# Optimization experiments

Measured on AMD Instinct MI355X. Metric: run time of the kernel, lower is better.

## Reference

```python
import jax, jax.numpy as jnp
import numpy as np

D_MODEL = 1024
N_HEAD = 16
D_K = D_MODEL // N_HEAD


def setup_inputs() -> dict:
    key = jax.random.key(0)
    ks = jax.random.split(key, 11)
    B, T = 2, 2048
    s = 1.0 / np.sqrt(D_MODEL)
    return {
        "q": jax.random.normal(ks[0], (B, T, D_MODEL), jnp.float32),
        "k": jax.random.normal(ks[1], (B, T, D_MODEL), jnp.float32),
        "v": jax.random.normal(ks[2], (B, T, D_MODEL), jnp.float32),
        "w_q": jax.random.normal(ks[3], (D_MODEL, D_MODEL), jnp.float32) * s,
        "b_q": jax.random.normal(ks[4], (D_MODEL,), jnp.float32) * 0.01,
        "w_k": jax.random.normal(ks[5], (D_MODEL, D_MODEL), jnp.float32) * s,
        "b_k": jax.random.normal(ks[6], (D_MODEL,), jnp.float32) * 0.01,
        "w_v": jax.random.normal(ks[7], (D_MODEL, D_MODEL), jnp.float32) * s,
        "b_v": jax.random.normal(ks[8], (D_MODEL,), jnp.float32) * 0.01,
        "w_o": jax.random.normal(ks[9], (D_MODEL, D_MODEL), jnp.float32) * s,
        "b_o": jax.random.normal(ks[10], (D_MODEL,), jnp.float32) * 0.01,
    }


def reference(q, k, v, w_q, b_q, w_k, b_k, w_v, b_v, w_o, b_o):
    B, T, _ = q.shape
    # QKV projections -> [B, H, T, d_k]
    def proj(x, w, b):
        return (jnp.einsum('btd,de->bte', x, w) + b).reshape(B, T, N_HEAD, D_K).transpose(0, 2, 1, 3)
    qh = proj(q, w_q, b_q)
    kh = proj(k, w_k, b_k)
    vh = proj(v, w_v, b_v)
    scale = jnp.float32(1.0 / np.sqrt(D_K))
    scores = jnp.einsum('bhqd,bhkd->bhqk', qh, kh) * scale  # [B,H,T,T]
    attn = jax.nn.softmax(scores, axis=-1)
    # dropout is identity in eval mode
    out = jnp.einsum('bhqk,bhkd->bhqd', attn, vh)  # [B,H,T,d_k]
    out = out.transpose(0, 2, 1, 3).reshape(B, T, N_HEAD * D_K)
    return jnp.einsum('btd,de->bte', out, w_o) + b_o
```

## Files before the change

### kernel.cpp

```cpp
#include <hip/hip_runtime.h>
#include <stdint.h>

#define DEVI static __device__ __forceinline__

typedef float f32x4 __attribute__((ext_vector_type(4)));
typedef float f32x16 __attribute__((ext_vector_type(16)));
typedef short s16x8 __attribute__((ext_vector_type(8)));
typedef unsigned short u16x4 __attribute__((ext_vector_type(4)));
typedef uint32_t u32x2 __attribute__((ext_vector_type(2)));
typedef uint32_t u32x4 __attribute__((ext_vector_type(4)));

DEVI unsigned short f2bf(float f) {
  union { float f; uint32_t u; } v; v.f = f;
  uint32_t u = v.u;
  return (unsigned short)((u + 0x7fffu + ((u >> 16) & 1u)) >> 16);
}

DEVI uint32_t cvtpk(float lo, float hi) {
  uint32_t r;
  asm("v_cvt_pk_bf16_f32 %0, %1, %2" : "=v"(r) : "v"(lo), "v"(hi));
  return r;
}

DEVI void pl32swap(uint32_t& a, uint32_t& b) {
#if __has_builtin(__builtin_amdgcn_permlane32_swap)
  u32x2 r = __builtin_amdgcn_permlane32_swap(a, b, false, false);
  a = r[0]; b = r[1];
#else
  asm("v_permlane32_swap_b32 %0, %1" : "+v"(a), "+v"(b));
#endif
}

DEVI void g2l16(const void* g, void* l) {
  __builtin_amdgcn_global_load_lds(
      (const __attribute__((address_space(1))) void*)g,
      (__attribute__((address_space(3))) void*)l, 16, 0, 0);
}

__global__ __launch_bounds__(256) void k_cvt3(const float* __restrict__ q,
                                              const float* __restrict__ k,
                                              const float* __restrict__ v,
                                              unsigned short* __restrict__ out) {
  const int y = blockIdx.y;
  const float* in = y == 0 ? q : y == 1 ? k : v;
  unsigned short* o = out + (size_t)y * 4194304;
  int idx = blockIdx.x * blockDim.x + threadIdx.x;
  int stride = gridDim.x * blockDim.x;
  for (int i = idx * 4; i < 4194304; i += stride * 4) {
    f32x4 x = *(const f32x4*)(in + i);
    u16x4 r;
    for (int j = 0; j < 4; ++j) r[j] = f2bf(x[j]);
    *(u16x4*)(o + i) = r;
  }
}

__global__ __launch_bounds__(256) void k_wt4(const float* w0, const float* w1,
                                             const float* w2, const float* w3,
                                             unsigned short* t0, unsigned short* t1,
                                             unsigned short* t2, unsigned short* t3) {
  const int z = blockIdx.z;
  const float* w = z == 0 ? w0 : z == 1 ? w1 : z == 2 ? w2 : w3;
  unsigned short* wt = z == 0 ? t0 : z == 1 ? t1 : z == 2 ? t2 : t3;
  __shared__ float tile[32][33];
  const int tx = threadIdx.x, ty = threadIdx.y;
  const int n0 = blockIdx.x * 32, k0 = blockIdx.y * 32;
  for (int j = 0; j < 4; ++j)
    tile[ty + j * 8][tx] = w[(size_t)(k0 + ty + j * 8) * 1024 + n0 + tx];
  __syncthreads();
  for (int j = 0; j < 4; ++j)
    wt[(size_t)(n0 + ty + j * 8) * 1024 + k0 + tx] = f2bf(tile[tx][ty + j * 8]);
}

__global__ __launch_bounds__(256) void k_gemm_multi(
    const unsigned short* A0, const unsigned short* A1, const unsigned short* A2,
    const unsigned short* B0, const unsigned short* B1, const unsigned short* B2,
    const float* c0, const float* c1, const float* c2,
    void* o0, void* o1, void* o2, int mode0) {
  constexpr int K = 1024;
  const int z = blockIdx.y;
  const unsigned short* A = z == 0 ? A0 : z == 1 ? A1 : A2;
  const unsigned short* Bt = z == 0 ? B0 : z == 1 ? B1 : B2;
  const float* bias = z == 0 ? c0 : z == 1 ? c1 : c2;
  void* outp = z == 0 ? o0 : z == 1 ? o1 : o2;
  const int MODE = mode0 + z;

  __shared__ __align__(16) unsigned short As[128 * 64];
  __shared__ __align__(16) unsigned short Bs[64 * 64];
  const int tid = threadIdx.x;
  const int lane = tid & 63, w = tid >> 6;
  const int g = lane >> 4, c = lane & 15;
  const int bm = blockIdx.x >> 4, bn = blockIdx.x & 15;
  const int m0 = bm * 128, n0 = bn * 64;
  const int wr = w >> 1, wc = w & 1;
  f32x4 acc[4][2] = {};

  for (int kt = 0; kt < 16; ++kt) {
    const int k0 = kt * 64;
    __syncthreads();
    for (int it = 0; it < 4; ++it) {
      int e = it * 256 + tid;
      int row = e >> 3, cwp = (e & 7) ^ (row & 7);
      g2l16(A + (size_t)(m0 + row) * K + k0 + cwp * 8,
            (char*)As + (it * 256 + (w << 6)) * 16);
    }
    for (int it = 0; it < 2; ++it) {
      int e = it * 256 + tid;
      int row = e >> 3, cwp = (e & 7) ^ (row & 7);
      g2l16(Bt + (size_t)(n0 + row) * K + k0 + cwp * 8,
            (char*)Bs + (it * 256 + (w << 6)) * 16);
    }
    __syncthreads();
    for (int kk = 0; kk < 2; ++kk) {
      s16x8 af[4], bfr[2];
      for (int mi = 0; mi < 4; ++mi) {
        int row = wr * 64 + mi * 16 + c;
        int ch = (kk * 4 + g) ^ (row & 7);
        af[mi] = *(const s16x8*)((const char*)As + row * 128 + ch * 16);
      }
      for (int ni = 0; ni < 2; ++ni) {
        int row = wc * 32 + ni * 16 + c;
        int ch = (kk * 4 + g) ^ (row & 7);
        bfr[ni] = *(const s16x8*)((const char*)Bs + row * 128 + ch * 16);
      }
      for (int mi = 0; mi < 4; ++mi)
        for (int ni = 0; ni < 2; ++ni)
          acc[mi][ni] = __builtin_amdgcn_mfma_f32_16x16x32_bf16(
              af[mi], bfr[ni], acc[mi][ni], 0, 0, 0);
    }
  }

  if (MODE == 0 || MODE == 1) {
    unsigned short* out = (unsigned short*)outp;
    const float scale = (MODE == 0) ? 0.1803368801111204f : 1.0f;
    for (int mi = 0; mi < 4; ++mi)
      for (int ni = 0; ni < 2; ++ni) {
        int row = m0 + wr * 64 + mi * 16 + g * 4;
        int col = n0 + wc * 32 + ni * 16 + c;
        float bb = bias[col];
        for (int r = 0; r < 4; ++r)
          out[(size_t)(row + r) * 1024 + col] = f2bf((acc[mi][ni][r] + bb) * scale);
      }
  } else if (MODE == 2) {
    unsigned short* vt = (unsigned short*)outp;
    const int bq = m0 >> 11, t0 = m0 & 2047;
    for (int mi = 0; mi < 4; ++mi)
      for (int ni = 0; ni < 2; ++ni) {
        int rowb = wr * 64 + mi * 16 + g * 4;
        int coll = wc * 32 + ni * 16 + c;
        float bb = bias[n0 + coll];
        u16x4 pk;
        for (int r = 0; r < 4; ++r) pk[r] = f2bf(acc[mi][ni][r] + bb);
        *(u16x4*)(vt + (size_t)(bq * 1024 + n0 + coll) * 2048 + t0 + rowb) = pk;
      }
  } else {
    float* out = (float*)outp;
    for (int mi = 0; mi < 4; ++mi)
      for (int ni = 0; ni < 2; ++ni) {
        int row = m0 + wr * 64 + mi * 16 + g * 4;
        int col = n0 + wc * 32 + ni * 16 + c;
        float bb = bias[col];
        for (int r = 0; r < 4; ++r)
          out[(size_t)(row + r) * 1024 + col] = acc[mi][ni][r] + bb;
      }
  }
}

__global__ __launch_bounds__(256) void k_attn(const unsigned short* __restrict__ Qp,
                                              const unsigned short* __restrict__ Kp,
                                              const unsigned short* __restrict__ Vt,
                                              unsigned short* __restrict__ Att) {
  __shared__ __align__(16) unsigned short Ks[2][4096];
  __shared__ __align__(16) unsigned short Vs[2][4096];
  const int tid = threadIdx.x;
  const int lane = tid & 63, w = tid >> 6;
  const int l31 = lane & 31, hi = lane >> 5;
  const int blk = (blockIdx.x & 7) * 64 + (blockIdx.x >> 3);
  const int qt = blk & 15, bh = blk >> 4;
  const int b = bh >> 4, h = bh & 15;
  const int m0 = qt * 128 + w * 32;
  const size_t qkBase = (size_t)b * 2048 * 1024 + (size_t)h * 64;
  const size_t vtBase = ((size_t)b * 1024 + h * 64) * 2048;

  const unsigned short* qrow = Qp + qkBase + (size_t)(m0 + l31) * 1024;
  s16x8 bq[4];
#pragma unroll
  for (int s = 0; s < 4; ++s)
    bq[s] = *(const s16x8*)(qrow + s * 16 + hi * 8);

  const int srow = tid >> 2;
  const unsigned short* kg = Kp + qkBase + (size_t)srow * 1024 + (tid & 3) * 16;
  const unsigned short* vg = Vt + vtBase + (size_t)srow * 2048 + (tid & 3) * 16;
  const int wof0 = srow * 128 + ((((tid & 3) * 2 + 0) ^ (srow & 7)) * 16);
  const int wof1 = srow * 128 + ((((tid & 3) * 2 + 1) ^ (srow & 7)) * 16);

  float m_run = -1e30f, l_run = 0.f;
  f32x16 o0 = {}, o1 = {};

  {
    s16x8 k0 = *(const s16x8*)(kg), k1 = *(const s16x8*)(kg + 8);
    s16x8 v0 = *(const s16x8*)(vg), v1 = *(const s16x8*)(vg + 8);
    *(s16x8*)((char*)&Ks[0][0] + wof0) = k0;
    *(s16x8*)((char*)&Ks[0][0] + wof1) = k1;
    *(s16x8*)((char*)&Vs[0][0] + wof0) = v0;
    *(s16x8*)((char*)&Vs[0][0] + wof1) = v1;
  }
  __syncthreads();

  const int rch = l31 & 7;

#pragma unroll 1
  for (int t = 0; t < 32; ++t) {
    const int cur = t & 1;
    s16x8 k0, k1, v0, v1;
    if (t < 31) {
      const unsigned short* kgt = kg + (size_t)(t + 1) * 64 * 1024;
      const unsigned short* vgt = vg + (t + 1) * 64;
      k0 = *(const s16x8*)(kgt);
      k1 = *(const s16x8*)(kgt + 8);
      v0 = *(const s16x8*)(vgt);
      v1 = *(const s16x8*)(vgt + 8);
    }
    const char* ks = (const char*)&Ks[cur][0];
    const char* vs = (const char*)&Vs[cur][0];

    f32x16 s0 = {}, s1 = {};
    __builtin_amdgcn_s_setprio(1);
#pragma unroll
    for (int ds = 0; ds < 4; ++ds) {
      int ch = (2 * ds + hi) ^ rch;
      s16x8 a0 = *(const s16x8*)(ks + l31 * 128 + ch * 16);
      s16x8 a1 = *(const s16x8*)(ks + (32 + l31) * 128 + ch * 16);
      s0 = __builtin_amdgcn_mfma_f32_32x32x16_bf16(a0, bq[ds], s0, 0, 0, 0);
      s1 = __builtin_amdgcn_mfma_f32_32x32x16_bf16(a1, bq[ds], s1, 0, 0, 0);
    }
    __builtin_amdgcn_s_setprio(0);

    float tm = s0[0];
#pragma unroll
    for (int j = 1; j < 16; ++j) tm = fmaxf(tm, s0[j]);
#pragma unroll
    for (int j = 0; j < 16; ++j) tm = fmaxf(tm, s1[j]);
    tm = fmaxf(tm, __shfl_xor(tm, 32));
    if (!__all(tm - m_run <= 8.0f)) {
      float mt = fmaxf(m_run, tm);
      float al = exp2f(m_run - mt);
      l_run *= al;
#pragma unroll
      for (int j = 0; j < 16; ++j) { o0[j] *= al; o1[j] *= al; }
      m_run = mt;
    }
    float rs = 0.f;
#pragma unroll
    for (int j = 0; j < 16; ++j) { float p = exp2f(s0[j] - m_run); s0[j] = p; rs += p; }
#pragma unroll
    for (int j = 0; j < 16; ++j) { float p = exp2f(s1[j] - m_run); s1[j] = p; rs += p; }
    rs += __shfl_xor(rs, 32);
    l_run += rs;

    s16x8 pf[4];
    {
      uint32_t w0 = cvtpk(s0[0], s0[1]), w1 = cvtpk(s0[2], s0[3]);
      uint32_t w2 = cvtpk(s0[4], s0[5]), w3 = cvtpk(s0[6], s0[7]);
      uint32_t w4 = cvtpk(s0[8], s0[9]), w5 = cvtpk(s0[10], s0[11]);
      uint32_t w6 = cvtpk(s0[12], s0[13]), w7 = cvtpk(s0[14], s0[15]);
      pl32swap(w0, w2); pl32swap(w1, w3); pl32swap(w4, w6); pl32swap(w5, w7);
      u32x4 f0 = {w0, w1, w2, w3}, f1 = {w4, w5, w6, w7};
      pf[0] = *(s16x8*)&f0;
      pf[1] = *(s16x8*)&f1;
    }
    {
      uint32_t w0 = cvtpk(s1[0], s1[1]), w1 = cvtpk(s1[2], s1[3]);
      uint32_t w2 = cvtpk(s1[4], s1[5]), w3 = cvtpk(s1[6], s1[7]);
      uint32_t w4 = cvtpk(s1[8], s1[9]), w5 = cvtpk(s1[10], s1[11]);
      uint32_t w6 = cvtpk(s1[12], s1[13]), w7 = cvtpk(s1[14], s1[15]);
      pl32swap(w0, w2); pl32swap(w1, w3); pl32swap(w4, w6); pl32swap(w5, w7);
      u32x4 f0 = {w0, w1, w2, w3}, f1 = {w4, w5, w6, w7};
      pf[2] = *(s16x8*)&f0;
      pf[3] = *(s16x8*)&f1;
    }

    __builtin_amdgcn_s_setprio(1);
#pragma unroll
    for (int ksp = 0; ksp < 4; ++ksp) {
      int ch = (2 * ksp + hi) ^ rch;
      s16x8 a0 = *(const s16x8*)(vs + l31 * 128 + ch * 16);
      s16x8 a1 = *(const s16x8*)(vs + (32 + l31) * 128 + ch * 16);
      o0 = __builtin_amdgcn_mfma_f32_32x32x16_bf16(a0, pf[ksp], o0, 0, 0, 0);
      o1 = __builtin_amdgcn_mfma_f32_32x32x16_bf16(a1, pf[ksp], o1, 0, 0, 0);
    }
    __builtin_amdgcn_s_setprio(0);

    if (t < 31) {
      const int nb = cur ^ 1;
      *(s16x8*)((char*)&Ks[nb][0] + wof0) = k0;
      *(s16x8*)((char*)&Ks[nb][0] + wof1) = k1;
      *(s16x8*)((char*)&Vs[nb][0] + wof0) = v0;
      *(s16x8*)((char*)&Vs[nb][0] + wof1) = v1;
    }
    __syncthreads();
  }

  float inv = 1.0f / l_run;
  unsigned short* arow = Att + ((size_t)b * 2048 + m0 + l31) * 1024 + h * 64;
#pragma unroll
  for (int dblk = 0; dblk < 2; ++dblk) {
#pragma unroll
    for (int rq = 0; rq < 4; ++rq) {
      float e0 = (dblk ? o1[rq * 4 + 0] : o0[rq * 4 + 0]) * inv;
      float e1 = (dblk ? o1[rq * 4 + 1] : o0[rq * 4 + 1]) * inv;
      float e2 = (dblk ? o1[rq * 4 + 2] : o0[rq * 4 + 2]) * inv;
      float e3 = (dblk ? o1[rq * 4 + 3] : o0[rq * 4 + 3]) * inv;
      u32x2 pk;
      pk[0] = cvtpk(e0, e1);
      pk[1] = cvtpk(e2, e3);
      *(u32x2*)(arow + dblk * 32 + 8 * rq + 4 * hi) = pk;
    }
  }
}

extern "C" void kernel_launch(void* const* d_in, const int* in_sizes, int n_in,
                              void* d_out, int out_size, void* d_ws, size_t ws_size,
                              hipStream_t stream) {
  const float* q = (const float*)d_in[0];
  const float* k = (const float*)d_in[1];
  const float* v = (const float*)d_in[2];
  const float* w_q = (const float*)d_in[3];
  const float* b_q = (const float*)d_in[4];
  const float* w_k = (const float*)d_in[5];
  const float* b_k = (const float*)d_in[6];
  const float* w_v = (const float*)d_in[7];
  const float* b_v = (const float*)d_in[8];
  const float* w_o = (const float*)d_in[9];
  const float* b_o = (const float*)d_in[10];

  unsigned short* s = (unsigned short*)d_ws;
  unsigned short* qbf = s;
  unsigned short* kbf = s + 4194304;
  unsigned short* vbf = s + 8388608;
  unsigned short* wqT = s + 12582912;
  unsigned short* wkT = s + 13631488;
  unsigned short* wvT = s + 14680064;
  unsigned short* woT = s + 15728640;
  unsigned short* Qp  = s + 16777216;
  unsigned short* Kp  = s + 20971520;
  unsigned short* Vt  = s + 25165824;
  unsigned short* Att = qbf;

  k_cvt3<<<dim3(1024, 3), 256, 0, stream>>>(q, k, v, qbf);

  k_wt4<<<dim3(32, 32, 4), dim3(32, 8), 0, stream>>>(w_q, w_k, w_v, w_o,
                                                     wqT, wkT, wvT, woT);

  k_gemm_multi<<<dim3(512, 3), 256, 0, stream>>>(
      qbf, kbf, vbf, wqT, wkT, wvT, b_q, b_k, b_v,
      (void*)Qp, (void*)Kp, (void*)Vt, 0);

  k_attn<<<512, 256, 0, stream>>>(Qp, Kp, Vt, Att);

  k_gemm_multi<<<dim3(512, 1), 256, 0, stream>>>(
      Att, Att, Att, woT, woT, woT, b_o, b_o, b_o,
      d_out, d_out, d_out, 3);
}
```

Measured before the change: 143.7 us.

## Fuse fp32-to-bf16 input conversion into QKV GEMM and halve attention block size

Removes the separate q/k/v conversion kernel by having the QKV GEMM load fp32 activations directly, convert them to bf16 in registers and store them into swizzled LDS. This drops one launch and a full write and re-read of the bf16 copies. It loses the async global-to-LDS path for A and re-reads fp32 once per N-tile. The attention kernel now runs 128-thread blocks over 64 query rows with twice as many blocks, each thread loading more K/V per tile. Softmax row sums are reduced across the half-wave once at the end via permlane swap, and the max/sum reductions use tree form.

```diff
diff --git a/kernel.cpp b/kernel.cpp
--- a/kernel.cpp
+++ b/kernel.cpp
@@ -31,27 +31,32 @@
 #endif
 }
 
+DEVI float swap_half(float x, int hi) {
+  uint32_t a = __float_as_uint(x), b = a;
+  pl32swap(a, b);
+  return hi ? __uint_as_float(a) : __uint_as_float(b);
+}
+
 DEVI void g2l16(const void* g, void* l) {
   __builtin_amdgcn_global_load_lds(
       (const __attribute__((address_space(1))) void*)g,
       (__attribute__((address_space(3))) void*)l, 16, 0, 0);
 }
 
-__global__ __launch_bounds__(256) void k_cvt3(const float* __restrict__ q,
-                                              const float* __restrict__ k,
-                                              const float* __restrict__ v,
-                                              unsigned short* __restrict__ out) {
-  const int y = blockIdx.y;
-  const float* in = y == 0 ? q : y == 1 ? k : v;
-  unsigned short* o = out + (size_t)y * 4194304;
-  int idx = blockIdx.x * blockDim.x + threadIdx.x;
-  int stride = gridDim.x * blockDim.x;
-  for (int i = idx * 4; i < 4194304; i += stride * 4) {
-    f32x4 x = *(const f32x4*)(in + i);
-    u16x4 r;
-    for (int j = 0; j < 4; ++j) r[j] = f2bf(x[j]);
-    *(u16x4*)(o + i) = r;
-  }
+DEVI float vmax16(const f32x16& v) {
+  float a = fmaxf(fmaxf(v[0], v[1]), fmaxf(v[2], v[3]));
+  float b = fmaxf(fmaxf(v[4], v[5]), fmaxf(v[6], v[7]));
+  float c = fmaxf(fmaxf(v[8], v[9]), fmaxf(v[10], v[11]));
+  float d = fmaxf(fmaxf(v[12], v[13]), fmaxf(v[14], v[15]));
+  return fmaxf(fmaxf(a, b), fmaxf(c, d));
+}
+
+DEVI float vsum16(const f32x16& v) {
+  float a = (v[0] + v[1]) + (v[2] + v[3]);
+  float b = (v[4] + v[5]) + (v[6] + v[7]);
+  float c = (v[8] + v[9]) + (v[10] + v[11]);
+  float d = (v[12] + v[13]) + (v[14] + v[15]);
+  return (a + b) + (c + d);
 }
 
 __global__ __launch_bounds__(256) void k_wt4(const float* w0, const float* w1,
@@ -71,14 +76,15 @@
     wt[(size_t)(n0 + ty + j * 8) * 1024 + k0 + tx] = f2bf(tile[tx][ty + j * 8]);
 }
 
+template <bool CVTA>
 __global__ __launch_bounds__(256) void k_gemm_multi(
-    const unsigned short* A0, const unsigned short* A1, const unsigned short* A2,
+    const void* A0, const void* A1, const void* A2,
     const unsigned short* B0, const unsigned short* B1, const unsigned short* B2,
     const float* c0, const float* c1, const float* c2,
     void* o0, void* o1, void* o2, int mode0) {
   constexpr int K = 1024;
   const int z = blockIdx.y;
-  const unsigned short* A = z == 0 ? A0 : z == 1 ? A1 : A2;
+  const void* Ap = z == 0 ? A0 : z == 1 ? A1 : A2;
   const unsigned short* Bt = z == 0 ? B0 : z == 1 ? B1 : B2;
   const float* bias = z == 0 ? c0 : z == 1 ? c1 : c2;
   void* outp = z == 0 ? o0 : z == 1 ? o1 : o2;
@@ -94,15 +100,38 @@
   const int wr = w >> 1, wc = w & 1;
   f32x4 acc[4][2] = {};
 
+  const int arow = tid >> 1, ahalf = tid & 1;
+
   for (int kt = 0; kt < 16; ++kt) {
     const int k0 = kt * 64;
     __syncthreads();
-    for (int it = 0; it < 4; ++it) {
-      int e = it * 256 + tid;
-      int row = e >> 3, cwp = (e & 7) ^ (row & 7);
-      g2l16(A + (size_t)(m0 + row) * K + k0 + cwp * 8,
-            (char*)As + (it * 256 + (w << 6)) * 16);
-    }
+    if constexpr (CVTA) {
+      const float* Af = (const float*)Ap;
+      const float* ag = Af + (size_t)(m0 + arow) * K + k0 + ahalf * 32;
+      f32x4 fa[8];
+#pragma unroll
+      for (int i = 0; i < 8; ++i) fa[i] = *(const f32x4*)(ag + i * 4);
+#pragma unroll
+      for (int j = 0; j < 4; ++j) {
+        u32x4 pk;
+        pk[0] = cvtpk(fa[2 * j][0], fa[2 * j][1]);
+        pk[1] = cvtpk(fa[2 * j][2], fa[2 * j][3]);
+        pk[2] = cvtpk(fa[2 * j + 1][0], fa[2 * j + 1][1]);
+        pk[3] = cvtpk(fa[2 * j + 1][2], fa[2 * j + 1][3]);
+        int cw = (ahalf * 4 + j) ^ (arow & 7);
+        *(u32x4*)((char*)As + arow * 128 + cw * 16) = pk;
+      }
+    } else {
+      const unsigned short* A = (const unsigned short*)Ap;
+#pragma unroll
+      for (int it = 0; it < 4; ++it) {
+        int e = it * 256 + tid;
+        int row = e >> 3, cwp = (e & 7) ^ (row & 7);
+        g2l16(A + (size_t)(m0 + row) * K + k0 + cwp * 8,
+              (char*)As + (it * 256 + (w << 6)) * 16);
+      }
+    }
+#pragma unroll
     for (int it = 0; it < 2; ++it) {
       int e = it * 256 + tid;
       int row = e >> 3, cwp = (e & 7) ^ (row & 7);
@@ -165,7 +194,7 @@
   }
 }
 
-__global__ __launch_bounds__(256) void k_attn(const unsigned short* __restrict__ Qp,
+__global__ __launch_bounds__(128) void k_attn(const unsigned short* __restrict__ Qp,
                                               const unsigned short* __restrict__ Kp,
                                               const unsigned short* __restrict__ Vt,
                                               unsigned short* __restrict__ Att) {
@@ -174,10 +203,10 @@
   const int tid = threadIdx.x;
   const int lane = tid & 63, w = tid >> 6;
   const int l31 = lane & 31, hi = lane >> 5;
-  const int blk = (blockIdx.x & 7) * 64 + (blockIdx.x >> 3);
-  const int qt = blk & 15, bh = blk >> 4;
+  const int blk = (blockIdx.x & 7) * 128 + (blockIdx.x >> 3);
+  const int qt = blk & 31, bh = blk >> 5;
   const int b = bh >> 4, h = bh & 15;
-  const int m0 = qt * 128 + w * 32;
+  const int m0 = qt * 64 + w * 32;
   const size_t qkBase = (size_t)b * 2048 * 1024 + (size_t)h * 64;
   const size_t vtBase = ((size_t)b * 1024 + h * 64) * 2048;
 
@@ -187,22 +216,30 @@
   for (int s = 0; s < 4; ++s)
     bq[s] = *(const s16x8*)(qrow + s * 16 + hi * 8);
 
-  const int srow = tid >> 2;
-  const unsigned short* kg = Kp + qkBase + (size_t)srow * 1024 + (tid & 3) * 16;
-  const unsigned short* vg = Vt + vtBase + (size_t)srow * 2048 + (tid & 3) * 16;
-  const int wof0 = srow * 128 + ((((tid & 3) * 2 + 0) ^ (srow & 7)) * 16);
-  const int wof1 = srow * 128 + ((((tid & 3) * 2 + 1) ^ (srow & 7)) * 16);
+  const int srow = tid >> 1, half = tid & 1;
+  const unsigned short* kg = Kp + qkBase + (size_t)srow * 1024 + half * 32;
+  const unsigned short* vg = Vt + vtBase + (size_t)srow * 2048 + half * 32;
+  int wof[4];
+#pragma unroll
+  for (int j = 0; j < 4; ++j)
+    wof[j] = srow * 128 + (((half * 4 + j) ^ (srow & 7)) * 16);
 
   float m_run = -1e30f, l_run = 0.f;
   f32x16 o0 = {}, o1 = {};
 
   {
     s16x8 k0 = *(const s16x8*)(kg), k1 = *(const s16x8*)(kg + 8);
+    s16x8 k2 = *(const s16x8*)(kg + 16), k3 = *(const s16x8*)(kg + 24);
     s16x8 v0 = *(const s16x8*)(vg), v1 = *(const s16x8*)(vg + 8);
-    *(s16x8*)((char*)&Ks[0][0] + wof0) = k0;
-    *(s16x8*)((char*)&Ks[0][0] + wof1) = k1;
-    *(s16x8*)((char*)&Vs[0][0] + wof0) = v0;
-    *(s16x8*)((char*)&Vs[0][0] + wof1) = v1;
+    s16x8 v2 = *(const s16x8*)(vg + 16), v3 = *(const s16x8*)(vg + 24);
+    *(s16x8*)((char*)&Ks[0][0] + wof[0]) = k0;
+    *(s16x8*)((char*)&Ks[0][0] + wof[1]) = k1;
+    *(s16x8*)((char*)&Ks[0][0] + wof[2]) = k2;
+    *(s16x8*)((char*)&Ks[0][0] + wof[3]) = k3;
+    *(s16x8*)((char*)&Vs[0][0] + wof[0]) = v0;
+    *(s16x8*)((char*)&Vs[0][0] + wof[1]) = v1;
+    *(s16x8*)((char*)&Vs[0][0] + wof[2]) = v2;
+    *(s16x8*)((char*)&Vs[0][0] + wof[3]) = v3;
   }
   __syncthreads();
 
@@ -211,14 +248,14 @@
 #pragma unroll 1
   for (int t = 0; t < 32; ++t) {
     const int cur = t & 1;
-    s16x8 k0, k1, v0, v1;
+    s16x8 k0, k1, k2, k3, v0, v1, v2, v3;
     if (t < 31) {
-      const unsigned short* kgt = kg + (size_t)(t + 1) * 64 * 1024;
+      const unsigned short* kgt = kg + (size_t)(t + 1) * 65536;
       const unsigned short* vgt = vg + (t + 1) * 64;
-      k0 = *(const s16x8*)(kgt);
-      k1 = *(const s16x8*)(kgt + 8);
-      v0 = *(const s16x8*)(vgt);
-      v1 = *(const s16x8*)(vgt + 8);
+      k0 = *(const s16x8*)(kgt);      k1 = *(const s16x8*)(kgt + 8);
+      k2 = *(const s16x8*)(kgt + 16); k3 = *(const s16x8*)(kgt + 24);
+      v0 = *(const s16x8*)(vgt);      v1 = *(const s16x8*)(vgt + 8);
+      v2 = *(const s16x8*)(vgt + 16); v3 = *(const s16x8*)(vgt + 24);
     }
     const char* ks = (const char*)&Ks[cur][0];
     const char* vs = (const char*)&Vs[cur][0];
@@ -235,12 +272,8 @@
     }
     __builtin_amdgcn_s_setprio(0);
 
-    float tm = s0[0];
-#pragma unroll
-    for (int j = 1; j < 16; ++j) tm = fmaxf(tm, s0[j]);
-#pragma unroll
-    for (int j = 0; j < 16; ++j) tm = fmaxf(tm, s1[j]);
-    tm = fmaxf(tm, __shfl_xor(tm, 32));
+    float tm = fmaxf(vmax16(s0), vmax16(s1));
+    tm = fmaxf(tm, swap_half(tm, hi));
     if (!__all(tm - m_run <= 8.0f)) {
       float mt = fmaxf(m_run, tm);
       float al = exp2f(m_run - mt);
@@ -249,13 +282,11 @@
       for (int j = 0; j < 16; ++j) { o0[j] *= al; o1[j] *= al; }
       m_run = mt;
     }
-    float rs = 0.f;
-#pragma unroll
-    for (int j = 0; j < 16; ++j) { float p = exp2f(s0[j] - m_run); s0[j] = p; rs += p; }
-#pragma unroll
-    for (int j = 0; j < 16; ++j) { float p = exp2f(s1[j] - m_run); s1[j] = p; rs += p; }
-    rs += __shfl_xor(rs, 32);
-    l_run += rs;
+#pragma unroll
+    for (int j = 0; j < 16; ++j) s0[j] = exp2f(s0[j] - m_run);
+#pragma unroll
+    for (int j = 0; j < 16; ++j) s1[j] = exp2f(s1[j] - m_run);
+    l_run += vsum16(s0) + vsum16(s1);
 
     s16x8 pf[4];
     {
@@ -292,15 +323,20 @@
 
     if (t < 31) {
       const int nb = cur ^ 1;
-      *(s16x8*)((char*)&Ks[nb][0] + wof0) = k0;
-      *(s16x8*)((char*)&Ks[nb][0] + wof1) = k1;
-      *(s16x8*)((char*)&Vs[nb][0] + wof0) = v0;
-      *(s16x8*)((char*)&Vs[nb][0] + wof1) = v1;
+      *(s16x8*)((char*)&Ks[nb][0] + wof[0]) = k0;
+      *(s16x8*)((char*)&Ks[nb][0] + wof[1]) = k1;
+      *(s16x8*)((char*)&Ks[nb][0] + wof[2]) = k2;
+      *(s16x8*)((char*)&Ks[nb][0] + wof[3]) = k3;
+      *(s16x8*)((char*)&Vs[nb][0] + wof[0]) = v0;
+      *(s16x8*)((char*)&Vs[nb][0] + wof[1]) = v1;
+      *(s16x8*)((char*)&Vs[nb][0] + wof[2]) = v2;
+      *(s16x8*)((char*)&Vs[nb][0] + wof[3]) = v3;
     }
     __syncthreads();
   }
 
-  float inv = 1.0f / l_run;
+  float lt = l_run + swap_half(l_run, hi);
+  float inv = 1.0f / lt;
   unsigned short* arow = Att + ((size_t)b * 2048 + m0 + l31) * 1024 + h * 64;
 #pragma unroll
   for (int dblk = 0; dblk < 2; ++dblk) {
@@ -334,9 +370,7 @@
   const float* b_o = (const float*)d_in[10];
 
   unsigned short* s = (unsigned short*)d_ws;
-  unsigned short* qbf = s;
-  unsigned short* kbf = s + 4194304;
-  unsigned short* vbf = s + 8388608;
+  unsigned short* Att = s;
   unsigned short* wqT = s + 12582912;
   unsigned short* wkT = s + 13631488;
   unsigned short* wvT = s + 14680064;
@@ -344,20 +378,17 @@
   unsigned short* Qp  = s + 16777216;
   unsigned short* Kp  = s + 20971520;
   unsigned short* Vt  = s + 25165824;
-  unsigned short* Att = qbf;
-
-  k_cvt3<<<dim3(1024, 3), 256, 0, stream>>>(q, k, v, qbf);
 
   k_wt4<<<dim3(32, 32, 4), dim3(32, 8), 0, stream>>>(w_q, w_k, w_v, w_o,
                                                      wqT, wkT, wvT, woT);
 
-  k_gemm_multi<<<dim3(512, 3), 256, 0, stream>>>(
-      qbf, kbf, vbf, wqT, wkT, wvT, b_q, b_k, b_v,
+  k_gemm_multi<true><<<dim3(512, 3), 256, 0, stream>>>(
+      q, k, v, wqT, wkT, wvT, b_q, b_k, b_v,
       (void*)Qp, (void*)Kp, (void*)Vt, 0);
 
-  k_attn<<<512, 256, 0, stream>>>(Qp, Kp, Vt, Att);
-
-  k_gemm_multi<<<dim3(512, 1), 256, 0, stream>>>(
+  k_attn<<<1024, 128, 0, stream>>>(Qp, Kp, Vt, Att);
+
+  k_gemm_multi<false><<<dim3(512, 1), 256, 0, stream>>>(
       Att, Att, Att, woT, woT, woT, b_o, b_o, b_o,
       d_out, d_out, d_out, 3);
 }
```

Measured after the change: 209.1 us. 45.5% more time.
